# Optimization experiments

Measured on AMD Instinct MI355X. Metric: run time of the kernel, lower is better.

The kernel has to match this reference:

```python
import jax, jax.numpy as jnp
import numpy as np
from jax import lax

H = 50  # hidden_size


def _lstm_layer(x, w_ih, w_hh, b_ih, b_hh):
    """Single LSTM layer, batch_first input x: [B, T, I]. PyTorch gate order i,f,g,o."""
    B = x.shape[0]
    # Precompute input projections for all timesteps: [B, T, 4H]
    x_proj = jnp.einsum('bti,gi->btg', x, w_ih) + b_ih + b_hh
    xs = jnp.swapaxes(x_proj, 0, 1)  # time-major [T, B, 4H]

    def step(carry, xp):
        h, c = carry
        gates = xp + h @ w_hh.T  # [B, 4H]
        i, f, g, o = jnp.split(gates, 4, axis=-1)
        i = jax.nn.sigmoid(i)
        f = jax.nn.sigmoid(f)
        g = jnp.tanh(g)
        o = jax.nn.sigmoid(o)
        c = f * c + i * g
        h = o * jnp.tanh(c)
        return (h, c), h

    h0 = jnp.zeros((B, H), dtype=x.dtype)
    c0 = jnp.zeros((B, H), dtype=x.dtype)
    (_, _), hs = lax.scan(step, (h0, c0), xs)
    return jnp.swapaxes(hs, 0, 1)  # back to [B, T, H]


def setup_inputs() -> dict:
    key = jax.random.key(0)
    ks = jax.random.split(key, 11)
    B, T = 512, 256
    I, O = 144, 144
    s = 0.1
    return {
        'x': jax.random.normal(ks[0], (B, T, 16, 9), dtype=jnp.float32),
        'w_ih0': jax.random.normal(ks[1], (4 * H, I), dtype=jnp.float32) * s,
        'w_hh0': jax.random.normal(ks[2], (4 * H, H), dtype=jnp.float32) * s,
        'b_ih0': jax.random.normal(ks[3], (4 * H,), dtype=jnp.float32) * s,
        'b_hh0': jax.random.normal(ks[4], (4 * H,), dtype=jnp.float32) * s,
        'w_ih1': jax.random.normal(ks[5], (4 * H, H), dtype=jnp.float32) * s,
        'w_hh1': jax.random.normal(ks[6], (4 * H, H), dtype=jnp.float32) * s,
        'b_ih1': jax.random.normal(ks[7], (4 * H,), dtype=jnp.float32) * s,
        'b_hh1': jax.random.normal(ks[8], (4 * H,), dtype=jnp.float32) * s,
        'w_fc': jax.random.normal(ks[9], (O, H), dtype=jnp.float32) * s,
        'b_fc': jax.random.normal(ks[10], (O,), dtype=jnp.float32) * s,
    }


def reference(x, w_ih0, w_hh0, b_ih0, b_hh0, w_ih1, w_hh1, b_ih1, b_hh1, w_fc, b_fc):
    B, T = x.shape[0], x.shape[1]
    x = x.reshape(B, T, -1)  # [B, T, 144]
    h1 = _lstm_layer(x, w_ih0, w_hh0, b_ih0, b_hh0)   # [B, T, H]
    h2 = _lstm_layer(h1, w_ih1, w_hh1, b_ih1, b_hh1)  # [B, T, H] (dropout inactive in eval)
    last = h2[:, -1, :]                               # [B, H]
    out = last @ w_fc.T + b_fc                        # [B, 144]
    return out.reshape(-1, 16, 9)
```

## Files before the change

kernel.cpp:

```cpp
#include <hip/hip_runtime.h>
#include <hip/hip_fp16.h>
#include <cstdint>
#include <cstddef>

#define H    50
#define TT   256
#define BATCH 512
#define KDIM 144
#define ODIM 144
#define NW   32
#define WS   8

typedef _Float16 half8  __attribute__((ext_vector_type(8)));
typedef _Float16 half4v __attribute__((ext_vector_type(4)));
typedef float    floatx4 __attribute__((ext_vector_type(4)));
typedef int      int4v  __attribute__((ext_vector_type(4)));

__device__ __forceinline__ float rcpf(float x) { return __builtin_amdgcn_rcpf(x); }
__device__ __forceinline__ float sigm(float x) { return rcpf(1.0f + __expf(-x)); }
__device__ __forceinline__ float tanhx(float x) {
    return 1.0f - 2.0f * rcpf(__expf(2.0f * x) + 1.0f);
}

__device__ __forceinline__ void sync_lds() {
    asm volatile("s_waitcnt lgkmcnt(0)\n\ts_barrier" ::: "memory");
}
__device__ __forceinline__ void wave_lds_fence() {
    asm volatile("s_waitcnt lgkmcnt(0)" ::: "memory");
}

__device__ __forceinline__ half8 make_hh(const float* __restrict__ Wt,
                                         int kkA, int gate, int q, int s) {
    const float* r0 = Wt + (size_t)(gate * H + (kkA < H ? kkA : 0)) * H;
    half8 r;
    #pragma unroll
    for (int j = 0; j < 8; ++j) {
        const int k = s * 32 + q * 8 + j;
        r[j] = (_Float16)((kkA < H && k < H) ? r0[k] : 0.0f);
    }
    return r;
}
__device__ __forceinline__ half8 make_ax(const float* __restrict__ Wih0,
                                         const float* __restrict__ bih0,
                                         const float* __restrict__ bhh0,
                                         int kkA, int gate, int q, int s) {
    const int p = gate * H + (kkA < H ? kkA : 0);
    half8 r;
    #pragma unroll
    for (int j = 0; j < 8; ++j) {
        const int k = s * 32 + q * 8 + j;
        float v = 0.0f;
        if (kkA < H) {
            if (k < KDIM)        v = Wih0[(size_t)p * KDIM + k];
            else if (k == KDIM)  v = bih0[p] + bhh0[p];
        }
        r[j] = (_Float16)v;
    }
    return r;
}
__device__ __forceinline__ half8 make_p1(const float* __restrict__ Wih1,
                                         const float* __restrict__ bih1,
                                         const float* __restrict__ bhh1,
                                         int kkA, int gate, int q, int s) {
    const int p = gate * H + (kkA < H ? kkA : 0);
    half8 r;
    #pragma unroll
    for (int j = 0; j < 8; ++j) {
        const int k = s * 32 + q * 8 + j;
        float v = 0.0f;
        if (kkA < H) {
            if (k < H)           v = Wih1[(size_t)p * H + k];
            else if (k == H)     v = bih1[p] + bhh1[p];
        }
        r[j] = (_Float16)v;
    }
    return r;
}

__global__ __launch_bounds__(256, 1) void lstm_fused(
    const float* __restrict__ X,
    const float* __restrict__ Whh0, const float* __restrict__ Wih0,
    const float* __restrict__ bih0, const float* __restrict__ bhh0,
    const float* __restrict__ Wih1, const float* __restrict__ Whh1,
    const float* __restrict__ bih1, const float* __restrict__ bhh1,
    const float* __restrict__ Wfc, const float* __restrict__ bfc,
    float* __restrict__ out)
{
    const int b0   = blockIdx.x * 2;
    const int tid  = threadIdx.x;
    const int lane = tid & 63;
    const int w    = tid >> 6;
    const int col  = lane & 15;
    const int q    = lane >> 4;

    __shared__ __align__(16) _Float16 B0[2][2][4][2][8];
    __shared__ __align__(16) _Float16 B1[2][2][4][2][8];
    __shared__ __align__(16) _Float16 HW[2][2][4][16][8];
    __shared__ __align__(16) float    gp0[64 * 72];
    __shared__ __align__(16) float    gp1[64 * 72];
    __shared__ __align__(16) _Float16 XB[2][5][4][16][8];
    __shared__ float h1f[2][52];

    int4v Ap[44];
    {
        const int prow = lane & 15;
        const int gate = prow & 3;
        #pragma unroll
        for (int tl = 0; tl < 4; ++tl) {
            const int kkA = 16 * w + 4 * tl + (prow >> 2);
            #pragma unroll
            for (int s = 0; s < 2; ++s) Ap[tl * 2 + s]      = __builtin_bit_cast(int4v, make_hh(Whh0, kkA, gate, q, s));
            #pragma unroll
            for (int s = 0; s < 5; ++s) Ap[8 + tl * 5 + s]  = __builtin_bit_cast(int4v, make_ax(Wih0, bih0, bhh0, kkA, gate, q, s));
            #pragma unroll
            for (int s = 0; s < 2; ++s) Ap[28 + tl * 2 + s] = __builtin_bit_cast(int4v, make_hh(Whh1, kkA, gate, q, s));
            #pragma unroll
            for (int s = 0; s < 2; ++s) Ap[36 + tl * 2 + s] = __builtin_bit_cast(int4v, make_p1(Wih1, bih1, bhh1, kkA, gate, q, s));
        }
    }
    #pragma unroll
    for (int i = 0; i < 44; ++i) asm volatile("" : "+a"(Ap[i]));

    const int  c2  = col >> 1;
    const int  r   = col & 1;
    const int  atl = c2 & 3;
    const int  aL  = c2 >> 2;
    const int  au  = 16 * w + 4 * atl + q;
    const bool areal = (au < H);
    float c = 0.0f;
    const float* gpb = (aL ? gp1 : gp0) + au * 72;

    const int cs1 = tid / 36,          kk1 = tid % 36;
    const int cs2 = (tid + 256) / 36,  kk2 = (tid + 256) % 36;
    const int cs3 = (tid + 512) / 36,  kk3 = (tid + 512) % 36;
    const float* xq1 = X + ((size_t)(b0 + (cs1 & 1)) * TT + (cs1 >> 1)) * KDIM + kk1 * 4;
    const float* xq2 = X + ((size_t)(b0 + (cs2 & 1)) * TT + (cs2 >> 1)) * KDIM + kk2 * 4;
    const float* xq3 = X + ((size_t)(b0 + (cs3 & 1)) * TT + (cs3 >> 1)) * KDIM + kk3 * 4;

    if (tid < 128) { ((int*)B0)[tid] = 0; ((int*)B1)[tid] = 0; }
    for (int i = tid; i < 1024; i += 256) ((int*)HW)[i] = 0;
    for (int i = tid; i < 2560; i += 256) ((int*)XB)[i] = 0;
    __syncthreads();
    if (tid < 32) {
        HW[tid >> 4][1][2][tid & 15][2] = (_Float16)1.0f;
        XB[tid >> 4][4][2][tid & 15][0] = (_Float16)1.0f;
    }
    {
        const float4 v1 = *(const float4*)xq1;
        half4v h; h[0]=(_Float16)v1.x; h[1]=(_Float16)v1.y; h[2]=(_Float16)v1.z; h[3]=(_Float16)v1.w;
        *(half4v*)&XB[0][kk1 >> 3][(kk1 >> 1) & 3][cs1][(kk1 & 1) * 4] = h;
        const float4 v2 = *(const float4*)xq2;
        half4v h2; h2[0]=(_Float16)v2.x; h2[1]=(_Float16)v2.y; h2[2]=(_Float16)v2.z; h2[3]=(_Float16)v2.w;
        *(half4v*)&XB[0][kk2 >> 3][(kk2 >> 1) & 3][cs2][(kk2 & 1) * 4] = h2;
        if (tid < 64) {
            const float4 v3 = *(const float4*)xq3;
            half4v h3; h3[0]=(_Float16)v3.x; h3[1]=(_Float16)v3.y; h3[2]=(_Float16)v3.z; h3[3]=(_Float16)v3.w;
            *(half4v*)&XB[0][kk3 >> 3][(kk3 >> 1) & 3][cs3][(kk3 & 1) * 4] = h3;
        }
    }
    __syncthreads();

    const int gb = (col >> 1) * 8 + (col & 1) * 4;

    for (int W = 0; W < NW; ++W) {
        #pragma unroll
        for (int i = 0; i < 44; ++i) asm volatile("" : "+a"(Ap[i]));
        const int cb = W & 1, nb = cb ^ 1, pb = cb ^ 1;
        const bool more = (W + 1) < NW;
        float4 xv1, xv2, xv3;
        if (more) {
            xv1 = *(const float4*)(xq1 + (size_t)(W + 1) * WS * KDIM);
            xv2 = *(const float4*)(xq2 + (size_t)(W + 1) * WS * KDIM);
            if (tid < 64) xv3 = *(const float4*)(xq3 + (size_t)(W + 1) * WS * KDIM);
        }
        {
            half8 xbf[5];
            #pragma unroll
            for (int s = 0; s < 5; ++s) xbf[s] = *(const half8*)&XB[cb][s][q][col][0];
            #pragma unroll
            for (int tl = 0; tl < 4; ++tl) {
                floatx4 px = (floatx4)(0.0f);
                #pragma unroll
                for (int s = 0; s < 5; ++s)
                    px = __builtin_amdgcn_mfma_f32_16x16x32_f16(__builtin_bit_cast(half8, Ap[8 + tl * 5 + s]), xbf[s], px, 0, 0, 0);
                *(floatx4*)&gp0[(16 * w + 4 * tl + q) * 72 + gb] = px;
            }
        }
        if (W > 0) {
            half8 hbf[2];
            #pragma unroll
            for (int s = 0; s < 2; ++s) hbf[s] = *(const half8*)&HW[pb][s][q][col][0];
            #pragma unroll
            for (int tl = 0; tl < 4; ++tl) {
                floatx4 pw = (floatx4)(0.0f);
                #pragma unroll
                for (int s = 0; s < 2; ++s)
                    pw = __builtin_amdgcn_mfma_f32_16x16x32_f16(__builtin_bit_cast(half8, Ap[36 + tl * 2 + s]), hbf[s], pw, 0, 0, 0);
                *(floatx4*)&gp1[(16 * w + 4 * tl + q) * 72 + gb] = pw;
            }
        }
        wave_lds_fence();
        #pragma unroll
        for (int i = 0; i < WS; ++i) {
            const int rb = i & 1, wb = rb ^ 1;
            half8 bf0[2], bf1[2];
            #pragma unroll
            for (int s = 0; s < 2; ++s) {
                bf0[s] = *(const half8*)&B0[rb][s][q][r][0];
                bf1[s] = *(const half8*)&B1[rb][s][q][r][0];
            }
            const floatx4 gx = *(const floatx4*)&gpb[i * 8 + r * 4];
            floatx4 a0[4], a1[4];
            #pragma unroll
            for (int tl = 0; tl < 4; ++tl) { a0[tl] = (floatx4)(0.0f); a1[tl] = (floatx4)(0.0f); }
            #pragma unroll
            for (int tl = 0; tl < 4; ++tl) {
                #pragma unroll
                for (int s = 0; s < 2; ++s) {
                    a0[tl] = __builtin_amdgcn_mfma_f32_16x16x32_f16(__builtin_bit_cast(half8, Ap[tl*2+s]),    bf0[s], a0[tl], 0, 0, 0);
                    a1[tl] = __builtin_amdgcn_mfma_f32_16x16x32_f16(__builtin_bit_cast(half8, Ap[28+tl*2+s]), bf1[s], a1[tl], 0, 0, 0);
                }
            }
            floatx4 g;
            #pragma unroll
            for (int gi_ = 0; gi_ < 4; ++gi_) {
                const float s01 = (c2 & 1) ? a0[1][gi_] : a0[0][gi_];
                const float s23 = (c2 & 1) ? a0[3][gi_] : a0[2][gi_];
                const float s45 = (c2 & 1) ? a1[1][gi_] : a1[0][gi_];
                const float s67 = (c2 & 1) ? a1[3][gi_] : a1[2][gi_];
                const float e0  = (c2 & 2) ? s23 : s01;
                const float e1  = (c2 & 2) ? s67 : s45;
                g[gi_] = (c2 & 4) ? e1 : e0;
            }
            if (aL == 0 || W > 0) {
                g[0] += gx[0]; g[1] += gx[1]; g[2] += gx[2]; g[3] += gx[3];
                const float gi = sigm(g[0]), gf = sigm(g[1]);
                const float gg = tanhx(g[2]), go = sigm(g[3]);
                c = gf * c + gi * gg;
                const float hv = go * tanhx(c);
                if (areal) {
                    const _Float16 h16 = (_Float16)hv;
                    if (aL == 0) {
                        B0[wb][au >> 5][(au >> 3) & 3][r][au & 7] = h16;
                        HW[cb][au >> 5][(au >> 3) & 3][2 * i + r][au & 7] = h16;
                    } else {
                        B1[wb][au >> 5][(au >> 3) & 3][r][au & 7] = h16;
                    }
                }
            }
            if (i == 3 && more) {
                half4v h; h[0]=(_Float16)xv1.x; h[1]=(_Float16)xv1.y; h[2]=(_Float16)xv1.z; h[3]=(_Float16)xv1.w;
                *(half4v*)&XB[nb][kk1 >> 3][(kk1 >> 1) & 3][cs1][(kk1 & 1) * 4] = h;
                half4v h2; h2[0]=(_Float16)xv2.x; h2[1]=(_Float16)xv2.y; h2[2]=(_Float16)xv2.z; h2[3]=(_Float16)xv2.w;
                *(half4v*)&XB[nb][kk2 >> 3][(kk2 >> 1) & 3][cs2][(kk2 & 1) * 4] = h2;
                if (tid < 64) {
                    half4v h3; h3[0]=(_Float16)xv3.x; h3[1]=(_Float16)xv3.y; h3[2]=(_Float16)xv3.z; h3[3]=(_Float16)xv3.w;
                    *(half4v*)&XB[nb][kk3 >> 3][(kk3 >> 1) & 3][cs3][(kk3 & 1) * 4] = h3;
                }
            }
            sync_lds();
        }
    }
    {
        #pragma unroll
        for (int i = 0; i < 44; ++i) asm volatile("" : "+a"(Ap[i]));
        {
            half8 hbf[2];
            #pragma unroll
            for (int s = 0; s < 2; ++s) hbf[s] = *(const half8*)&HW[(NW - 1) & 1][s][q][col][0];
            #pragma unroll
            for (int tl = 0; tl < 4; ++tl) {
                floatx4 pw = (floatx4)(0.0f);
                #pragma unroll
                for (int s = 0; s < 2; ++s)
                    pw = __builtin_amdgcn_mfma_f32_16x16x32_f16(__builtin_bit_cast(half8, Ap[36 + tl * 2 + s]), hbf[s], pw, 0, 0, 0);
                *(floatx4*)&gp1[(16 * w + 4 * tl + q) * 72 + gb] = pw;
            }
        }
        wave_lds_fence();
        #pragma unroll
        for (int i = 0; i < WS; ++i) {
            const int rb = i & 1, wb = rb ^ 1;
            half8 bf1[2];
            #pragma unroll
            for (int s = 0; s < 2; ++s) bf1[s] = *(const half8*)&B1[rb][s][q][r][0];
            const floatx4 gx = *(const floatx4*)&gpb[i * 8 + r * 4];
            floatx4 a1[4];
            #pragma unroll
            for (int tl = 0; tl < 4; ++tl) {
                a1[tl] = (floatx4)(0.0f);
                #pragma unroll
                for (int s = 0; s < 2; ++s)
                    a1[tl] = __builtin_amdgcn_mfma_f32_16x16x32_f16(__builtin_bit_cast(half8, Ap[28+tl*2+s]), bf1[s], a1[tl], 0, 0, 0);
            }
            if (aL == 1) {
                floatx4 g;
                #pragma unroll
                for (int gi_ = 0; gi_ < 4; ++gi_) {
                    const float s01 = (c2 & 1) ? a1[1][gi_] : a1[0][gi_];
                    const float s23 = (c2 & 1) ? a1[3][gi_] : a1[2][gi_];
                    g[gi_] = (c2 & 2) ? s23 : s01;
                }
                g[0] += gx[0]; g[1] += gx[1]; g[2] += gx[2]; g[3] += gx[3];
                const float gi = sigm(g[0]), gf = sigm(g[1]);
                const float gg = tanhx(g[2]), go = sigm(g[3]);
                c = gf * c + gi * gg;
                const float hv = go * tanhx(c);
                if (areal) {
                    B1[wb][au >> 5][(au >> 3) & 3][r][au & 7] = (_Float16)hv;
                    if (i == WS - 1) h1f[r][au] = hv;
                }
            }
            sync_lds();
        }
    }
    for (int oo = tid; oo < 2 * ODIM; oo += 256) {
        const int rr = oo / ODIM, o = oo - rr * ODIM;
        float s = bfc[o];
        const float* wr = Wfc + (size_t)o * H;
        #pragma unroll
        for (int k = 0; k < H; ++k) s += wr[k] * h1f[rr][k];
        out[(size_t)(b0 + rr) * ODIM + o] = s;
    }
}

extern "C" void kernel_launch(void* const* d_in, const int* in_sizes, int n_in,
                              void* d_out, int out_size, void* d_ws, size_t ws_size,
                              hipStream_t stream) {
    const float* x    = (const float*)d_in[0];
    const float* wih0 = (const float*)d_in[1];
    const float* whh0 = (const float*)d_in[2];
    const float* bih0 = (const float*)d_in[3];
    const float* bhh0 = (const float*)d_in[4];
    const float* wih1 = (const float*)d_in[5];
    const float* whh1 = (const float*)d_in[6];
    const float* bih1 = (const float*)d_in[7];
    const float* bhh1 = (const float*)d_in[8];
    const float* wfc  = (const float*)d_in[9];
    const float* bfc  = (const float*)d_in[10];
    float* outp = (float*)d_out;

    lstm_fused<<<BATCH / 2, 256, 0, stream>>>(x, whh0, wih0, bih0, bhh0,
                                              wih1, whh1, bih1, bhh1,
                                              wfc, bfc, outp);
}
```

Measured before the change: 309.0 us.

## Process one batch row per block and allow two blocks per CU

Each block now handles a single sequence instead of two, so the launch has twice as many blocks, and launch bounds are raised to allow two resident blocks per CU. Layer-0 hidden state is read directly from the HW staging buffer, which removes the separate B0 buffer, and the LDS buffers are halved. The aim is to fill more CUs and overlap the latency-bound recurrent steps of two blocks per CU. In exchange, half of each MFMA's columns now do redundant work, and the tighter register budget for two blocks per CU may cause spills of the 44 AGPR-resident weight fragments.

```diff
diff --git a/kernel.cpp b/kernel.cpp
--- a/kernel.cpp
+++ b/kernel.cpp
@@ -77,7 +77,7 @@
     return r;
 }
 
-__global__ __launch_bounds__(256, 1) void lstm_fused(
+__global__ __launch_bounds__(256, 2) void lstm_fused(
     const float* __restrict__ X,
     const float* __restrict__ Whh0, const float* __restrict__ Wih0,
     const float* __restrict__ bih0, const float* __restrict__ bhh0,
@@ -86,20 +86,19 @@
     const float* __restrict__ Wfc, const float* __restrict__ bfc,
     float* __restrict__ out)
 {
-    const int b0   = blockIdx.x * 2;
+    const int b    = blockIdx.x;
     const int tid  = threadIdx.x;
     const int lane = tid & 63;
     const int w    = tid >> 6;
     const int col  = lane & 15;
     const int q    = lane >> 4;
 
-    __shared__ __align__(16) _Float16 B0[2][2][4][2][8];
-    __shared__ __align__(16) _Float16 B1[2][2][4][2][8];
-    __shared__ __align__(16) _Float16 HW[2][2][4][16][8];
-    __shared__ __align__(16) float    gp0[64 * 72];
-    __shared__ __align__(16) float    gp1[64 * 72];
-    __shared__ __align__(16) _Float16 XB[2][5][4][16][8];
-    __shared__ float h1f[2][52];
+    __shared__ __align__(16) _Float16 B1[2][2][4][8];
+    __shared__ __align__(16) _Float16 HW[2][2][4][8][8];
+    __shared__ __align__(16) _Float16 XB[2][5][4][8][8];
+    __shared__ __align__(16) float    gp0[64 * 36];
+    __shared__ __align__(16) float    gp1[64 * 36];
+    __shared__ float h1f[52];
 
     int4v Ap[44];
     {
@@ -122,94 +121,92 @@
     for (int i = 0; i < 44; ++i) asm volatile("" : "+a"(Ap[i]));
 
     const int  c2  = col >> 1;
-    const int  r   = col & 1;
     const int  atl = c2 & 3;
     const int  aL  = c2 >> 2;
     const int  au  = 16 * w + 4 * atl + q;
+    const bool valid = ((col & 1) == 0);
     const bool areal = (au < H);
     float c = 0.0f;
-    const float* gpb = (aL ? gp1 : gp0) + au * 72;
-
-    const int cs1 = tid / 36,          kk1 = tid % 36;
-    const int cs2 = (tid + 256) / 36,  kk2 = (tid + 256) % 36;
-    const int cs3 = (tid + 512) / 36,  kk3 = (tid + 512) % 36;
-    const float* xq1 = X + ((size_t)(b0 + (cs1 & 1)) * TT + (cs1 >> 1)) * KDIM + kk1 * 4;
-    const float* xq2 = X + ((size_t)(b0 + (cs2 & 1)) * TT + (cs2 >> 1)) * KDIM + kk2 * 4;
-    const float* xq3 = X + ((size_t)(b0 + (cs3 & 1)) * TT + (cs3 >> 1)) * KDIM + kk3 * 4;
-
-    if (tid < 128) { ((int*)B0)[tid] = 0; ((int*)B1)[tid] = 0; }
-    for (int i = tid; i < 1024; i += 256) ((int*)HW)[i] = 0;
-    for (int i = tid; i < 2560; i += 256) ((int*)XB)[i] = 0;
+    const float* gpb = (aL ? gp1 : gp0) + au * 36;
+
+    const int cs1 = tid / 36,         kk1 = tid % 36;
+    const int cs2 = (tid + 256) / 36, kk2 = (tid + 256) % 36;
+    const float* xq1 = X + ((size_t)b * TT + cs1) * KDIM + kk1 * 4;
+    const float* xq2 = X + ((size_t)b * TT + cs2) * KDIM + kk2 * 4;
+
+    if (tid < 64) ((int*)B1)[tid] = 0;
+    for (int i = tid; i < 512; i += 256) ((int*)HW)[i] = 0;
+    for (int i = tid; i < 1280; i += 256) ((int*)XB)[i] = 0;
+    for (int i = tid; i < 2304; i += 256) gp1[i] = 0.0f;
     __syncthreads();
-    if (tid < 32) {
-        HW[tid >> 4][1][2][tid & 15][2] = (_Float16)1.0f;
-        XB[tid >> 4][4][2][tid & 15][0] = (_Float16)1.0f;
-    }
+    if (tid < 16) {
+        HW[tid >> 3][1][2][tid & 7][2] = (_Float16)1.0f;
+        XB[tid >> 3][4][2][tid & 7][0] = (_Float16)1.0f;
+    }
+    __syncthreads();
     {
         const float4 v1 = *(const float4*)xq1;
         half4v h; h[0]=(_Float16)v1.x; h[1]=(_Float16)v1.y; h[2]=(_Float16)v1.z; h[3]=(_Float16)v1.w;
         *(half4v*)&XB[0][kk1 >> 3][(kk1 >> 1) & 3][cs1][(kk1 & 1) * 4] = h;
-        const float4 v2 = *(const float4*)xq2;
-        half4v h2; h2[0]=(_Float16)v2.x; h2[1]=(_Float16)v2.y; h2[2]=(_Float16)v2.z; h2[3]=(_Float16)v2.w;
-        *(half4v*)&XB[0][kk2 >> 3][(kk2 >> 1) & 3][cs2][(kk2 & 1) * 4] = h2;
-        if (tid < 64) {
-            const float4 v3 = *(const float4*)xq3;
-            half4v h3; h3[0]=(_Float16)v3.x; h3[1]=(_Float16)v3.y; h3[2]=(_Float16)v3.z; h3[3]=(_Float16)v3.w;
-            *(half4v*)&XB[0][kk3 >> 3][(kk3 >> 1) & 3][cs3][(kk3 & 1) * 4] = h3;
+        if (tid < 32) {
+            const float4 v2 = *(const float4*)xq2;
+            half4v h2; h2[0]=(_Float16)v2.x; h2[1]=(_Float16)v2.y; h2[2]=(_Float16)v2.z; h2[3]=(_Float16)v2.w;
+            *(half4v*)&XB[0][kk2 >> 3][(kk2 >> 1) & 3][cs2][(kk2 & 1) * 4] = h2;
         }
     }
     __syncthreads();
-
-    const int gb = (col >> 1) * 8 + (col & 1) * 4;
 
     for (int W = 0; W < NW; ++W) {
         #pragma unroll
         for (int i = 0; i < 44; ++i) asm volatile("" : "+a"(Ap[i]));
         const int cb = W & 1, nb = cb ^ 1, pb = cb ^ 1;
         const bool more = (W + 1) < NW;
-        float4 xv1, xv2, xv3;
+        float4 xv1, xv2;
         if (more) {
             xv1 = *(const float4*)(xq1 + (size_t)(W + 1) * WS * KDIM);
-            xv2 = *(const float4*)(xq2 + (size_t)(W + 1) * WS * KDIM);
-            if (tid < 64) xv3 = *(const float4*)(xq3 + (size_t)(W + 1) * WS * KDIM);
+            if (tid < 32) xv2 = *(const float4*)(xq2 + (size_t)(W + 1) * WS * KDIM);
         }
         {
             half8 xbf[5];
             #pragma unroll
-            for (int s = 0; s < 5; ++s) xbf[s] = *(const half8*)&XB[cb][s][q][col][0];
+            for (int s = 0; s < 5; ++s) xbf[s] = *(const half8*)&XB[cb][s][q][col & 7][0];
             #pragma unroll
             for (int tl = 0; tl < 4; ++tl) {
                 floatx4 px = (floatx4)(0.0f);
                 #pragma unroll
                 for (int s = 0; s < 5; ++s)
                     px = __builtin_amdgcn_mfma_f32_16x16x32_f16(__builtin_bit_cast(half8, Ap[8 + tl * 5 + s]), xbf[s], px, 0, 0, 0);
-                *(floatx4*)&gp0[(16 * w + 4 * tl + q) * 72 + gb] = px;
+                if (col < 8)
+                    *(floatx4*)&gp0[(16 * w + 4 * tl + q) * 36 + col * 4] = px;
             }
         }
         if (W > 0) {
             half8 hbf[2];
             #pragma unroll
-            for (int s = 0; s < 2; ++s) hbf[s] = *(const half8*)&HW[pb][s][q][col][0];
+            for (int s = 0; s < 2; ++s) hbf[s] = *(const half8*)&HW[pb][s][q][col & 7][0];
             #pragma unroll
             for (int tl = 0; tl < 4; ++tl) {
                 floatx4 pw = (floatx4)(0.0f);
                 #pragma unroll
                 for (int s = 0; s < 2; ++s)
                     pw = __builtin_amdgcn_mfma_f32_16x16x32_f16(__builtin_bit_cast(half8, Ap[36 + tl * 2 + s]), hbf[s], pw, 0, 0, 0);
-                *(floatx4*)&gp1[(16 * w + 4 * tl + q) * 72 + gb] = pw;
+                if (col < 8)
+                    *(floatx4*)&gp1[(16 * w + 4 * tl + q) * 36 + col * 4] = pw;
             }
         }
         wave_lds_fence();
         #pragma unroll
         for (int i = 0; i < WS; ++i) {
             const int rb = i & 1, wb = rb ^ 1;
+            const int b0i = (i == 0) ? pb : cb;
+            const int tprev = (i == 0) ? 7 : (i - 1);
             half8 bf0[2], bf1[2];
             #pragma unroll
             for (int s = 0; s < 2; ++s) {
-                bf0[s] = *(const half8*)&B0[rb][s][q][r][0];
-                bf1[s] = *(const half8*)&B1[rb][s][q][r][0];
-            }
-            const floatx4 gx = *(const floatx4*)&gpb[i * 8 + r * 4];
+                bf0[s] = *(const half8*)&HW[b0i][s][q][tprev][0];
+                bf1[s] = *(const half8*)&B1[rb][s][q][0];
+            }
+            const floatx4 gx = *(const floatx4*)&gpb[i * 4];
             floatx4 a0[4], a1[4];
             #pragma unroll
             for (int tl = 0; tl < 4; ++tl) { a0[tl] = (floatx4)(0.0f); a1[tl] = (floatx4)(0.0f); }
@@ -224,38 +221,34 @@
             floatx4 g;
             #pragma unroll
             for (int gi_ = 0; gi_ < 4; ++gi_) {
-                const float s01 = (c2 & 1) ? a0[1][gi_] : a0[0][gi_];
-                const float s23 = (c2 & 1) ? a0[3][gi_] : a0[2][gi_];
-                const float s45 = (c2 & 1) ? a1[1][gi_] : a1[0][gi_];
-                const float s67 = (c2 & 1) ? a1[3][gi_] : a1[2][gi_];
-                const float e0  = (c2 & 2) ? s23 : s01;
-                const float e1  = (c2 & 2) ? s67 : s45;
+                const float s01a = (c2 & 1) ? a0[1][gi_] : a0[0][gi_];
+                const float s23a = (c2 & 1) ? a0[3][gi_] : a0[2][gi_];
+                const float s01b = (c2 & 1) ? a1[1][gi_] : a1[0][gi_];
+                const float s23b = (c2 & 1) ? a1[3][gi_] : a1[2][gi_];
+                const float e0 = (c2 & 2) ? s23a : s01a;
+                const float e1 = (c2 & 2) ? s23b : s01b;
                 g[gi_] = (c2 & 4) ? e1 : e0;
             }
-            if (aL == 0 || W > 0) {
-                g[0] += gx[0]; g[1] += gx[1]; g[2] += gx[2]; g[3] += gx[3];
-                const float gi = sigm(g[0]), gf = sigm(g[1]);
-                const float gg = tanhx(g[2]), go = sigm(g[3]);
-                c = gf * c + gi * gg;
-                const float hv = go * tanhx(c);
-                if (areal) {
-                    const _Float16 h16 = (_Float16)hv;
-                    if (aL == 0) {
-                        B0[wb][au >> 5][(au >> 3) & 3][r][au & 7] = h16;
-                        HW[cb][au >> 5][(au >> 3) & 3][2 * i + r][au & 7] = h16;
-                    } else {
-                        B1[wb][au >> 5][(au >> 3) & 3][r][au & 7] = h16;
-                    }
-                }
+            g[0] += gx[0]; g[1] += gx[1]; g[2] += gx[2]; g[3] += gx[3];
+            const float gi = sigm(g[0]), gf = sigm(g[1]);
+            const float gg = tanhx(g[2]), go = sigm(g[3]);
+            const bool en = (aL == 0) || (W > 0);
+            const float cn = gf * c + gi * gg;
+            c = en ? cn : c;
+            const float hv = go * tanhx(c);
+            if (valid && areal && en) {
+                const _Float16 h16 = (_Float16)hv;
+                if (aL == 0)
+                    HW[cb][au >> 5][(au >> 3) & 3][i][au & 7] = h16;
+                else
+                    B1[wb][au >> 5][(au >> 3) & 3][au & 7] = h16;
             }
             if (i == 3 && more) {
                 half4v h; h[0]=(_Float16)xv1.x; h[1]=(_Float16)xv1.y; h[2]=(_Float16)xv1.z; h[3]=(_Float16)xv1.w;
                 *(half4v*)&XB[nb][kk1 >> 3][(kk1 >> 1) & 3][cs1][(kk1 & 1) * 4] = h;
-                half4v h2; h2[0]=(_Float16)xv2.x; h2[1]=(_Float16)xv2.y; h2[2]=(_Float16)xv2.z; h2[3]=(_Float16)xv2.w;
-                *(half4v*)&XB[nb][kk2 >> 3][(kk2 >> 1) & 3][cs2][(kk2 & 1) * 4] = h2;
-                if (tid < 64) {
-                    half4v h3; h3[0]=(_Float16)xv3.x; h3[1]=(_Float16)xv3.y; h3[2]=(_Float16)xv3.z; h3[3]=(_Float16)xv3.w;
-                    *(half4v*)&XB[nb][kk3 >> 3][(kk3 >> 1) & 3][cs3][(kk3 & 1) * 4] = h3;
+                if (tid < 32) {
+                    half4v h2; h2[0]=(_Float16)xv2.x; h2[1]=(_Float16)xv2.y; h2[2]=(_Float16)xv2.z; h2[3]=(_Float16)xv2.w;
+                    *(half4v*)&XB[nb][kk2 >> 3][(kk2 >> 1) & 3][cs2][(kk2 & 1) * 4] = h2;
                 }
             }
             sync_lds();
@@ -267,14 +260,15 @@
         {
             half8 hbf[2];
             #pragma unroll
-            for (int s = 0; s < 2; ++s) hbf[s] = *(const half8*)&HW[(NW - 1) & 1][s][q][col][0];
+            for (int s = 0; s < 2; ++s) hbf[s] = *(const half8*)&HW[(NW - 1) & 1][s][q][col & 7][0];
             #pragma unroll
             for (int tl = 0; tl < 4; ++tl) {
                 floatx4 pw = (floatx4)(0.0f);
                 #pragma unroll
                 for (int s = 0; s < 2; ++s)
                     pw = __builtin_amdgcn_mfma_f32_16x16x32_f16(__builtin_bit_cast(half8, Ap[36 + tl * 2 + s]), hbf[s], pw, 0, 0, 0);
-                *(floatx4*)&gp1[(16 * w + 4 * tl + q) * 72 + gb] = pw;
+                if (col < 8)
+                    *(floatx4*)&gp1[(16 * w + 4 * tl + q) * 36 + col * 4] = pw;
             }
         }
         wave_lds_fence();
@@ -283,8 +277,8 @@
             const int rb = i & 1, wb = rb ^ 1;
             half8 bf1[2];
             #pragma unroll
-            for (int s = 0; s < 2; ++s) bf1[s] = *(const half8*)&B1[rb][s][q][r][0];
-            const floatx4 gx = *(const floatx4*)&gpb[i * 8 + r * 4];
+            for (int s = 0; s < 2; ++s) bf1[s] = *(const half8*)&B1[rb][s][q][0];
+            const floatx4 gx = *(const floatx4*)&gpb[i * 4];
             floatx4 a1[4];
             #pragma unroll
             for (int tl = 0; tl < 4; ++tl) {
@@ -293,34 +287,33 @@
                 for (int s = 0; s < 2; ++s)
                     a1[tl] = __builtin_amdgcn_mfma_f32_16x16x32_f16(__builtin_bit_cast(half8, Ap[28+tl*2+s]), bf1[s], a1[tl], 0, 0, 0);
             }
-            if (aL == 1) {
-                floatx4 g;
-                #pragma unroll
-                for (int gi_ = 0; gi_ < 4; ++gi_) {
-                    const float s01 = (c2 & 1) ? a1[1][gi_] : a1[0][gi_];
-                    const float s23 = (c2 & 1) ? a1[3][gi_] : a1[2][gi_];
-                    g[gi_] = (c2 & 2) ? s23 : s01;
-                }
-                g[0] += gx[0]; g[1] += gx[1]; g[2] += gx[2]; g[3] += gx[3];
-                const float gi = sigm(g[0]), gf = sigm(g[1]);
-                const float gg = tanhx(g[2]), go = sigm(g[3]);
-                c = gf * c + gi * gg;
-                const float hv = go * tanhx(c);
-                if (areal) {
-                    B1[wb][au >> 5][(au >> 3) & 3][r][au & 7] = (_Float16)hv;
-                    if (i == WS - 1) h1f[r][au] = hv;
-                }
+            floatx4 g;
+            #pragma unroll
+            for (int gi_ = 0; gi_ < 4; ++gi_) {
+                const float s01 = (c2 & 1) ? a1[1][gi_] : a1[0][gi_];
+                const float s23 = (c2 & 1) ? a1[3][gi_] : a1[2][gi_];
+                g[gi_] = (c2 & 2) ? s23 : s01;
+            }
+            g[0] += gx[0]; g[1] += gx[1]; g[2] += gx[2]; g[3] += gx[3];
+            const float gi = sigm(g[0]), gf = sigm(g[1]);
+            const float gg = tanhx(g[2]), go = sigm(g[3]);
+            const bool en = (aL == 1);
+            const float cn = gf * c + gi * gg;
+            c = en ? cn : c;
+            const float hv = go * tanhx(c);
+            if (valid && en && areal) {
+                B1[wb][au >> 5][(au >> 3) & 3][au & 7] = (_Float16)hv;
+                if (i == WS - 1) h1f[au] = hv;
             }
             sync_lds();
         }
     }
-    for (int oo = tid; oo < 2 * ODIM; oo += 256) {
-        const int rr = oo / ODIM, o = oo - rr * ODIM;
-        float s = bfc[o];
-        const float* wr = Wfc + (size_t)o * H;
-        #pragma unroll
-        for (int k = 0; k < H; ++k) s += wr[k] * h1f[rr][k];
-        out[(size_t)(b0 + rr) * ODIM + o] = s;
+    if (tid < ODIM) {
+        float s = bfc[tid];
+        const float* wr = Wfc + (size_t)tid * H;
+        #pragma unroll
+        for (int k = 0; k < H; ++k) s += wr[k] * h1f[k];
+        out[(size_t)b * ODIM + tid] = s;
     }
 }
 
@@ -340,7 +333,7 @@
     const float* bfc  = (const float*)d_in[10];
     float* outp = (float*)d_out;
 
-    lstm_fused<<<BATCH / 2, 256, 0, stream>>>(x, whh0, wih0, bih0, bhh0,
-                                              wih1, whh1, bih1, bhh1,
-                                              wfc, bfc, outp);
-}
+    lstm_fused<<<BATCH, 256, 0, stream>>>(x, whh0, wih0, bih0, bhh0,
+                                          wih1, whh1, bih1, bhh1,
+                                          wfc, bfc, outp);
+}
```

New measurement: 481.8 us. 1.56x slower.
